# Optimization experiments

Measured on AMD Instinct MI355X. Metric: run time of the kernel, lower is better.

## Reference

```python
import jax, jax.numpy as jnp
import numpy as np

B, C, W, H = 2, 64, 96, 96


def _conv1x1(Wm, b, x):
    # 1x1 conv == per-pixel channel mixing: (O,C) x (B,C,W,H) -> (B,O,W,H)
    return jnp.einsum('oc,bchw->bohw', Wm, x) + b[None, :, None, None]


def setup_inputs() -> dict:
    key = jax.random.key(0)
    ks = jax.random.split(key, 12)
    s = 1.0 / np.sqrt(C)
    inp = {
        'x': jax.random.normal(ks[0], (B, C, W, H), jnp.float32),
        'y': jax.random.normal(ks[1], (B, C, W, H), jnp.float32),
        'Wq': jax.random.normal(ks[2], (C, C), jnp.float32) * s,
        'bq': jax.random.normal(ks[3], (C,), jnp.float32) * 0.01,
        'Wk': jax.random.normal(ks[4], (C, C), jnp.float32) * s,
        'bk': jax.random.normal(ks[5], (C,), jnp.float32) * 0.01,
        'Wvx': jax.random.normal(ks[6], (C, C), jnp.float32) * s,
        'bvx': jax.random.normal(ks[7], (C,), jnp.float32) * 0.01,
        'Wvy': jax.random.normal(ks[8], (C, C), jnp.float32) * s,
        'bvy': jax.random.normal(ks[9], (C,), jnp.float32) * 0.01,
        'gamma': jax.random.normal(ks[10], (1,), jnp.float32) * 0.1,
        'beta': jax.random.normal(ks[11], (1,), jnp.float32) * 0.1,
    }
    return inp


def reference(x, y, Wq, bq, Wk, bk, Wvx, bvx, Wvy, bvy, gamma, beta):
    b, c, w, h = x.shape
    n = w * h
    # Q from y, K from x (cross-query structure of the original module)
    q = _conv1x1(Wq, bq, y).reshape(b, c, n)          # (B,C,N)
    k = _conv1x1(Wk, bk, x).reshape(b, c, n)          # (B,C,N)
    energy = jnp.einsum('bcm,bcn->bmn', q, k)         # (B,N,N), query rows m
    attention = jax.nn.softmax(energy, axis=-1)       # softmax over keys n
    vx = _conv1x1(Wvx, bvx, x).reshape(b, c, n)       # (B,C,N)
    vy = _conv1x1(Wvy, bvy, y).reshape(b, c, n)
    # torch: bmm(value, attention^T) -> out[:, :, m] = sum_n value[:, :, n] * att[m, n]
    out_x = jnp.einsum('bcn,bmn->bcm', vx, attention).reshape(b, c, w, h)
    out_y = jnp.einsum('bcn,bmn->bcm', vy, attention).reshape(b, c, w, h)
    x_att = gamma[0] * out_x
    y_att = beta[0] * out_y
    return (x_att, y_att)
```

## Files before the change

### kernel.cpp

```cpp
#include <hip/hip_runtime.h>
#include <cstdint>
#include <cstddef>

#define BN 2
#define CC 64
#define NN 9216
#define KT 64
#define L2E 1.44269504088896340736f
#define M0L2 63.478581798f
#define PPAD 72

typedef __attribute__((ext_vector_type(8))) _Float16 half8;
typedef __attribute__((ext_vector_type(2))) __fp16 fp16x2;
typedef __attribute__((ext_vector_type(8))) short s16x8;
typedef __attribute__((ext_vector_type(4))) float f32x4;
typedef unsigned short u16;
typedef unsigned int u32;

__device__ __forceinline__ u16 f2h(float f) {
  union { _Float16 h; u16 u; } c; c.h = (_Float16)f; return c.u;
}
__device__ __forceinline__ u32 pack2h(float a, float b) {
  return (u32)f2h(a) | ((u32)f2h(b) << 16);
}
__device__ __forceinline__ u16 f2bf(float f) {
  union { float f; u32 u; } c; c.f = f;
  u32 u = c.u + 0x7FFFu + ((c.u >> 16) & 1u);
  return (u16)(u >> 16);
}
__device__ __forceinline__ half8 cvt8(f32x4 lo, f32x4 hi) {
  union { half8 v; fp16x2 p[4]; } u;
  u.p[0] = __builtin_amdgcn_cvt_pkrtz(lo[0], lo[1]);
  u.p[1] = __builtin_amdgcn_cvt_pkrtz(lo[2], lo[3]);
  u.p[2] = __builtin_amdgcn_cvt_pkrtz(hi[0], hi[1]);
  u.p[3] = __builtin_amdgcn_cvt_pkrtz(hi[2], hi[3]);
  return u.v;
}
__device__ __forceinline__ u32 fbits(float f) {
  union { float f; u32 u; } c; c.f = f; return c.u;
}
__device__ __forceinline__ void cp16(const u16* g, u16* l) {
  __builtin_amdgcn_global_load_lds(
      (const __attribute__((address_space(1))) u32*)g,
      (__attribute__((address_space(3))) u32*)l, 16, 0, 0);
}

__global__ __launch_bounds__(256) void conv_mfma_kernel(
    const float* __restrict__ x, const float* __restrict__ y,
    const float* __restrict__ Wq, const float* __restrict__ bq,
    const float* __restrict__ Wk, const float* __restrict__ bk,
    const float* __restrict__ Wvx, const float* __restrict__ bvx,
    const float* __restrict__ Wvy, const float* __restrict__ bvy,
    u16* __restrict__ qkv) {
  const int cv = blockIdx.y;
  const int b = blockIdx.z;
  const int p0 = blockIdx.x * 128;
  const int tid = threadIdx.x;
  const int lane = tid & 63;
  const int wv = tid >> 6;
  const int l15 = lane & 15;
  const int h = lane >> 4;

  const float* src = (cv == 1 || cv == 2) ? x : y;
  const float* Wm = cv == 0 ? Wq : (cv == 1 ? Wk : (cv == 2 ? Wvx : Wvy));
  const float* bv = cv == 0 ? bq : (cv == 1 ? bk : (cv == 2 ? bvx : bvy));
  u16* dst = qkv + (size_t)cv * ((size_t)BN * NN * CC);

  __shared__ u16 Tr[128 * 72];

  half8 wf[4][2];
#pragma unroll
  for (int ob = 0; ob < 4; ++ob)
#pragma unroll
    for (int kc = 0; kc < 2; ++kc) {
      const float* wr = Wm + (16 * ob + l15) * 64 + 32 * kc + 8 * h;
      wf[ob][kc] = cvt8(*(const f32x4*)wr, *(const f32x4*)(wr + 4));
    }

  f32x4 acc[2][4];
#pragma unroll
  for (int ob = 0; ob < 4; ++ob) {
    f32x4 bias = *(const f32x4*)(bv + 16 * ob + 4 * h);
#pragma unroll
    for (int pt = 0; pt < 2; ++pt) acc[pt][ob] = bias;
  }

  const float* xbase = src + (size_t)b * CC * NN;
#pragma unroll
  for (int pt = 0; pt < 2; ++pt) {
    const int px = p0 + 32 * wv + 16 * pt + l15;
    half8 xf[2];
#pragma unroll
    for (int kc = 0; kc < 2; ++kc) {
      const float* xp = xbase + (size_t)(32 * kc + 8 * h) * NN + px;
      float s[8];
#pragma unroll
      for (int j = 0; j < 8; ++j) s[j] = xp[(size_t)j * NN];
      xf[kc] = cvt8((f32x4){s[0], s[1], s[2], s[3]},
                    (f32x4){s[4], s[5], s[6], s[7]});
    }
#pragma unroll
    for (int ob = 0; ob < 4; ++ob) {
      acc[pt][ob] = __builtin_amdgcn_mfma_f32_16x16x32_f16(wf[ob][0], xf[0], acc[pt][ob], 0, 0, 0);
      acc[pt][ob] = __builtin_amdgcn_mfma_f32_16x16x32_f16(wf[ob][1], xf[1], acc[pt][ob], 0, 0, 0);
    }
  }

  if (cv >= 2) {
#pragma unroll
    for (int pt = 0; pt < 2; ++pt)
#pragma unroll
      for (int ob = 0; ob < 4; ++ob)
#pragma unroll
        for (int r = 0; r < 4; ++r)
          dst[((size_t)b * CC + 16 * ob + 4 * h + r) * NN +
              p0 + 32 * wv + 16 * pt + l15] = f2bf(acc[pt][ob][r]);
  } else {
#pragma unroll
    for (int pt = 0; pt < 2; ++pt) {
      const int pxl = 32 * wv + 16 * pt + l15;
#pragma unroll
      for (int ob = 0; ob < 4; ++ob) {
        uint2 v;
        v.x = pack2h(acc[pt][ob][0], acc[pt][ob][1]);
        v.y = pack2h(acc[pt][ob][2], acc[pt][ob][3]);
        *(uint2*)(Tr + pxl * 72 + 16 * ob + 4 * h) = v;
      }
    }
    __syncthreads();
    const int row = tid >> 1;
    const int hf = tid & 1;
    const uint4* s4 = (const uint4*)(Tr + row * 72) + hf * 4;
    uint4* d4 = (uint4*)(dst + ((size_t)b * NN + p0 + row) * CC) + hf * 4;
#pragma unroll
    for (int i = 0; i < 4; ++i) d4[i] = s4[i];
  }
}

#define TILE_OFF(R, c0) ((((R) * 8) + ((c0) ^ ((R) & 7))) * 8)

template <int SP>
__global__ __launch_bounds__(256, 3) void flash_kernel(
    const u16* __restrict__ qkv, float* __restrict__ accX,
    float* __restrict__ accY, float* __restrict__ ml) {
  constexpr int KPS = NN / SP;
  constexpr int STEPS = KPS / KT;
  const int tid = threadIdx.x;
  const int lane = tid & 63;
  const int wv = tid >> 6;
  const int l15 = lane & 15;
  const int h = lane >> 4;
  const int s = blockIdx.y;
  const int b = blockIdx.z;
  const int m0w = blockIdx.x * 128 + wv * 32;

  const u16* Qt = qkv;
  const u16* Kt = qkv + (size_t)1 * BN * NN * CC;
  const u16* Vx = qkv + (size_t)2 * BN * NN * CC;
  const u16* Vy = qkv + (size_t)3 * BN * NN * CC;

  __shared__ u16 Klds[2][64 * 64];
  __shared__ u16 Vxlds[64 * 64];
  __shared__ u16 Vylds[64 * 64];
  __shared__ u16 Plds[4][32 * PPAD];

  {
    const int n0 = s * KPS;
#pragma unroll
    for (int it = 0; it < 2; ++it) {
      int i = tid + it * 256;
      int r = i >> 3, cc = i & 7;
      int sc = (cc ^ (r & 7)) * 8;
      cp16(Kt + ((size_t)b * NN + n0 + r) * CC + sc, (u16*)Klds[0] + (size_t)i * 8);
    }
  }

  half8 qf[2][2];
#pragma unroll
  for (int mb = 0; mb < 2; ++mb)
#pragma unroll
    for (int ch = 0; ch < 2; ++ch)
      qf[mb][ch] = *(const half8*)(Qt + ((size_t)b * NN + m0w + 16 * mb + l15) * CC +
                                   32 * ch + 8 * h);

  const s16x8 ones = {0x3F80, 0x3F80, 0x3F80, 0x3F80,
                      0x3F80, 0x3F80, 0x3F80, 0x3F80};

  f32x4 oX[4][2], oY[4][2], lacc[2];
#pragma unroll
  for (int cb = 0; cb < 4; ++cb)
#pragma unroll
    for (int mb = 0; mb < 2; ++mb) {
      oX[cb][mb] = (f32x4){0.f, 0.f, 0.f, 0.f};
      oY[cb][mb] = (f32x4){0.f, 0.f, 0.f, 0.f};
    }
#pragma unroll
  for (int mb = 0; mb < 2; ++mb) lacc[mb] = (f32x4){0.f, 0.f, 0.f, 0.f};

  __syncthreads();

  int kb = 0;
#pragma unroll 1
  for (int step = 0; step < STEPS; ++step) {
    const int n0 = s * KPS + step * KT;

#pragma unroll
    for (int it = 0; it < 2; ++it) {
      int i = tid + it * 256;
      int r = i >> 3, cc = i & 7;
      int sc = (cc ^ (r & 7)) * 8;
      cp16(Vx + ((size_t)b * CC + r) * NN + n0 + sc, (u16*)Vxlds + (size_t)i * 8);
      cp16(Vy + ((size_t)b * CC + r) * NN + n0 + sc, (u16*)Vylds + (size_t)i * 8);
    }
    if (step + 1 < STEPS) {
      const int n1 = n0 + KT;
#pragma unroll
      for (int it = 0; it < 2; ++it) {
        int i = tid + it * 256;
        int r = i >> 3, cc = i & 7;
        int sc = (cc ^ (r & 7)) * 8;
        cp16(Kt + ((size_t)b * NN + n1 + r) * CC + sc,
             (u16*)Klds[kb ^ 1] + (size_t)i * 8);
      }
      asm volatile("s_waitcnt vmcnt(6)" ::: "memory");
    } else {
      asm volatile("s_waitcnt vmcnt(4)" ::: "memory");
    }
    __builtin_amdgcn_s_barrier();
    asm volatile("" ::: "memory");

    half8 kf[4][2];
#pragma unroll
    for (int nb = 0; nb < 4; ++nb) {
      int R = 16 * nb + l15;
#pragma unroll
      for (int ch = 0; ch < 2; ++ch)
        kf[nb][ch] = *(const half8*)((const u16*)Klds[kb] + TILE_OFF(R, 4 * ch + h));
    }
    f32x4 st[2][4];
    __builtin_amdgcn_s_setprio(1);
#pragma unroll
    for (int mb = 0; mb < 2; ++mb)
#pragma unroll
      for (int nb = 0; nb < 4; ++nb) {
        f32x4 a = (f32x4){0.f, 0.f, 0.f, 0.f};
        a = __builtin_amdgcn_mfma_f32_16x16x32_f16(kf[nb][0], qf[mb][0], a, 0, 0, 0);
        a = __builtin_amdgcn_mfma_f32_16x16x32_f16(kf[nb][1], qf[mb][1], a, 0, 0, 0);
        st[mb][nb] = a;
      }
    __builtin_amdgcn_s_setprio(0);

#pragma unroll
    for (int mb = 0; mb < 2; ++mb) {
      u32* prow = (u32*)(&Plds[wv][(16 * mb + l15) * PPAD]);
#pragma unroll
      for (int nb = 0; nb < 4; ++nb) {
        u32 u0 = fbits(exp2f(fmaf(st[mb][nb][0], L2E, -M0L2)));
        u32 u1 = fbits(exp2f(fmaf(st[mb][nb][1], L2E, -M0L2)));
        u32 u2 = fbits(exp2f(fmaf(st[mb][nb][2], L2E, -M0L2)));
        u32 u3 = fbits(exp2f(fmaf(st[mb][nb][3], L2E, -M0L2)));
        uint2 v;
        v.x = (u0 >> 16) | (u1 & 0xffff0000u);
        v.y = (u2 >> 16) | (u3 & 0xffff0000u);
        *(uint2*)(prow + 8 * nb + 2 * h) = v;
      }
    }

    asm volatile("s_waitcnt lgkmcnt(0)" ::: "memory");

    s16x8 pf[2][2];
#pragma unroll
    for (int mb = 0; mb < 2; ++mb) {
      int R = 16 * mb + l15;
#pragma unroll
      for (int kc = 0; kc < 2; ++kc)
        pf[mb][kc] = *(const s16x8*)(&Plds[wv][0] + R * PPAD + (4 * kc + h) * 8);
    }

    if (step + 1 < STEPS) {
      asm volatile("s_waitcnt vmcnt(2)" ::: "memory");
    } else {
      asm volatile("s_waitcnt vmcnt(0)" ::: "memory");
    }
    __builtin_amdgcn_s_barrier();
    asm volatile("" ::: "memory");

    __builtin_amdgcn_s_setprio(1);
#pragma unroll
    for (int cb = 0; cb < 4; ++cb) {
      int R = 16 * cb + l15;
#pragma unroll
      for (int kc = 0; kc < 2; ++kc) {
        s16x8 bx = *(const s16x8*)(Vxlds + TILE_OFF(R, 4 * kc + h));
        s16x8 by = *(const s16x8*)(Vylds + TILE_OFF(R, 4 * kc + h));
#pragma unroll
        for (int mb = 0; mb < 2; ++mb) {
          oX[cb][mb] = __builtin_amdgcn_mfma_f32_16x16x32_bf16(pf[mb][kc], bx, oX[cb][mb], 0, 0, 0);
          oY[cb][mb] = __builtin_amdgcn_mfma_f32_16x16x32_bf16(pf[mb][kc], by, oY[cb][mb], 0, 0, 0);
        }
      }
    }
#pragma unroll
    for (int mb = 0; mb < 2; ++mb)
#pragma unroll
      for (int kc = 0; kc < 2; ++kc)
        lacc[mb] = __builtin_amdgcn_mfma_f32_16x16x32_bf16(pf[mb][kc], ones, lacc[mb], 0, 0, 0);
    __builtin_amdgcn_s_setprio(0);

    __builtin_amdgcn_s_barrier();
    asm volatile("" ::: "memory");
    kb ^= 1;
  }

  const size_t bs = (size_t)b * SP + s;
#pragma unroll
  for (int mb = 0; mb < 2; ++mb) {
#pragma unroll
    for (int r = 0; r < 4; ++r) {
      const int m = m0w + 16 * mb + 4 * h + r;
      if (l15 == 0) ml[bs * NN + m] = lacc[mb][r];
#pragma unroll
      for (int cb = 0; cb < 4; ++cb) {
        accX[(bs * NN + m) * CC + 16 * cb + l15] = oX[cb][mb][r];
        accY[(bs * NN + m) * CC + 16 * cb + l15] = oY[cb][mb][r];
      }
    }
  }
}

template <int SP>
__global__ __launch_bounds__(256) void combine_kernel(
    const float* __restrict__ accX, const float* __restrict__ accY,
    const float* __restrict__ ml, const float* __restrict__ gbuf,
    const float* __restrict__ bbuf, float* __restrict__ out) {
  const int tid = threadIdx.x;
  const int b = blockIdx.x / 288;
  const int m0 = (blockIdx.x % 288) * 32;
  __shared__ float lX[64][33];
  __shared__ float lY[64][33];
  {
    const int mi = tid >> 3;
    const int c0 = (tid & 7) * 8;
    const int m = m0 + mi;
    float L = 0.f;
#pragma unroll
    for (int sp = 0; sp < SP; ++sp)
      L += ml[((size_t)b * SP + sp) * NN + m];
    const float invL = 1.0f / L;
    const float ga = gbuf[0] * invL;
    const float be = bbuf[0] * invL;
    f32x4 xv0 = (f32x4){0.f, 0.f, 0.f, 0.f}, xv1 = xv0, yv0 = xv0, yv1 = xv0;
#pragma unroll
    for (int sp = 0; sp < SP; ++sp) {
      size_t off = (((size_t)b * SP + sp) * NN + m) * CC + c0;
      xv0 += *(const f32x4*)(accX + off);
      xv1 += *(const f32x4*)(accX + off + 4);
      yv0 += *(const f32x4*)(accY + off);
      yv1 += *(const f32x4*)(accY + off + 4);
    }
#pragma unroll
    for (int r = 0; r < 4; ++r) {
      lX[c0 + r][mi] = xv0[r] * ga;
      lX[c0 + 4 + r][mi] = xv1[r] * ga;
      lY[c0 + r][mi] = yv0[r] * be;
      lY[c0 + 4 + r][mi] = yv1[r] * be;
    }
  }
  __syncthreads();
  {
    const int c = tid >> 2;
    const int mq = (tid & 3) * 8;
    float* ox = out + ((size_t)b * CC + c) * NN + m0 + mq;
    float* oy = ox + (size_t)BN * CC * NN;
    f32x4 vx0, vx1, vy0, vy1;
#pragma unroll
    for (int r = 0; r < 4; ++r) {
      vx0[r] = lX[c][mq + r];
      vx1[r] = lX[c][mq + 4 + r];
      vy0[r] = lY[c][mq + r];
      vy1[r] = lY[c][mq + 4 + r];
    }
    *(f32x4*)ox = vx0;
    *(f32x4*)(ox + 4) = vx1;
    *(f32x4*)oy = vy0;
    *(f32x4*)(oy + 4) = vy1;
  }
}

extern "C" void kernel_launch(void* const* d_in, const int* in_sizes, int n_in,
                              void* d_out, int out_size, void* d_ws, size_t ws_size,
                              hipStream_t stream) {
  const float* x   = (const float*)d_in[0];
  const float* y   = (const float*)d_in[1];
  const float* Wq  = (const float*)d_in[2];
  const float* bq  = (const float*)d_in[3];
  const float* Wk  = (const float*)d_in[4];
  const float* bk  = (const float*)d_in[5];
  const float* Wvx = (const float*)d_in[6];
  const float* bvx = (const float*)d_in[7];
  const float* Wvy = (const float*)d_in[8];
  const float* bvy = (const float*)d_in[9];
  const float* ga  = (const float*)d_in[10];
  const float* be  = (const float*)d_in[11];

  const size_t qkv_bytes = (size_t)4 * BN * NN * CC * 2;

  conv_mfma_kernel<<<dim3(72, 4, 2), 256, 0, stream>>>(x, y, Wq, bq, Wk, bk,
                                                       Wvx, bvx, Wvy, bvy,
                                                       (u16*)d_ws);

  const size_t acc8 = (size_t)BN * 8 * NN * CC * 4;
  const size_t need8 = qkv_bytes + 2 * acc8 + (size_t)BN * 8 * NN * 4;

  u16* qkv = (u16*)d_ws;
  if (ws_size >= need8) {
    float* accX = (float*)((char*)d_ws + qkv_bytes);
    float* accY = accX + (size_t)BN * 8 * NN * CC;
    float* mlb  = accY + (size_t)BN * 8 * NN * CC;
    flash_kernel<8><<<dim3(72, 8, BN), 256, 0, stream>>>(qkv, accX, accY, mlb);
    combine_kernel<8><<<dim3(576), 256, 0, stream>>>(accX, accY, mlb, ga, be,
                                                     (float*)d_out);
  } else {
    float* accX = (float*)((char*)d_ws + qkv_bytes);
    float* accY = accX + (size_t)BN * 4 * NN * CC;
    float* mlb  = accY + (size_t)BN * 4 * NN * CC;
    flash_kernel<4><<<dim3(72, 4, BN), 256, 0, stream>>>(qkv, accX, accY, mlb);
    combine_kernel<4><<<dim3(576), 256, 0, stream>>>(accX, accY, mlb, ga, be,
                                                     (float*)d_out);
  }
}
```

Baseline: 207.7 us.

## Permute K rows so QK^T MFMA output feeds PV operand directly from registers

Loads K tiles into LDS with a permuted row order, so the score accumulator layout from the QK^T MFMA already matches the A-operand layout the PV MFMA expects. This removes the per-wave P staging buffer in LDS, along with its writes, the lgkmcnt wait and the reads back. The freed LDS and registers allow the occupancy hint to rise from 3 to 5 blocks per CU. Correctness depends on the permutation matching both MFMA layouts exactly, and the higher occupancy target may cause register spills.

```diff
diff --git a/kernel.cpp b/kernel.cpp
--- a/kernel.cpp
+++ b/kernel.cpp
@@ -8,7 +8,6 @@
 #define KT 64
 #define L2E 1.44269504088896340736f
 #define M0L2 63.478581798f
-#define PPAD 72
 
 typedef __attribute__((ext_vector_type(8))) _Float16 half8;
 typedef __attribute__((ext_vector_type(2))) __fp16 fp16x2;
@@ -43,6 +42,9 @@
   __builtin_amdgcn_global_load_lds(
       (const __attribute__((address_space(1))) u32*)g,
       (__attribute__((address_space(3))) u32*)l, 16, 0, 0);
+}
+__device__ __forceinline__ int permk(int r) {
+  return (r & 0x23) | ((r & 0x0C) << 1) | ((r & 0x10) >> 2);
 }
 
 __global__ __launch_bounds__(256) void conv_mfma_kernel(
@@ -140,7 +142,7 @@
 #define TILE_OFF(R, c0) ((((R) * 8) + ((c0) ^ ((R) & 7))) * 8)
 
 template <int SP>
-__global__ __launch_bounds__(256, 3) void flash_kernel(
+__global__ __launch_bounds__(256, 5) void flash_kernel(
     const u16* __restrict__ qkv, float* __restrict__ accX,
     float* __restrict__ accY, float* __restrict__ ml) {
   constexpr int KPS = NN / SP;
@@ -162,7 +164,6 @@
   __shared__ u16 Klds[2][64 * 64];
   __shared__ u16 Vxlds[64 * 64];
   __shared__ u16 Vylds[64 * 64];
-  __shared__ u16 Plds[4][32 * PPAD];
 
   {
     const int n0 = s * KPS;
@@ -171,7 +172,8 @@
       int i = tid + it * 256;
       int r = i >> 3, cc = i & 7;
       int sc = (cc ^ (r & 7)) * 8;
-      cp16(Kt + ((size_t)b * NN + n0 + r) * CC + sc, (u16*)Klds[0] + (size_t)i * 8);
+      cp16(Kt + ((size_t)b * NN + n0 + permk(r)) * CC + sc,
+           (u16*)Klds[0] + (size_t)i * 8);
     }
   }
 
@@ -219,7 +221,7 @@
         int i = tid + it * 256;
         int r = i >> 3, cc = i & 7;
         int sc = (cc ^ (r & 7)) * 8;
-        cp16(Kt + ((size_t)b * NN + n1 + r) * CC + sc,
+        cp16(Kt + ((size_t)b * NN + n1 + permk(r)) * CC + sc,
              (u16*)Klds[kb ^ 1] + (size_t)i * 8);
       }
       asm volatile("s_waitcnt vmcnt(6)" ::: "memory");
@@ -250,31 +252,28 @@
       }
     __builtin_amdgcn_s_setprio(0);
 
+    s16x8 pf[2][2];
 #pragma unroll
     for (int mb = 0; mb < 2; ++mb) {
-      u32* prow = (u32*)(&Plds[wv][(16 * mb + l15) * PPAD]);
+      uint2 pw[4];
 #pragma unroll
       for (int nb = 0; nb < 4; ++nb) {
         u32 u0 = fbits(exp2f(fmaf(st[mb][nb][0], L2E, -M0L2)));
         u32 u1 = fbits(exp2f(fmaf(st[mb][nb][1], L2E, -M0L2)));
         u32 u2 = fbits(exp2f(fmaf(st[mb][nb][2], L2E, -M0L2)));
         u32 u3 = fbits(exp2f(fmaf(st[mb][nb][3], L2E, -M0L2)));
-        uint2 v;
-        v.x = (u0 >> 16) | (u1 & 0xffff0000u);
-        v.y = (u2 >> 16) | (u3 & 0xffff0000u);
-        *(uint2*)(prow + 8 * nb + 2 * h) = v;
-      }
-    }
-
-    asm volatile("s_waitcnt lgkmcnt(0)" ::: "memory");
-
-    s16x8 pf[2][2];
-#pragma unroll
-    for (int mb = 0; mb < 2; ++mb) {
-      int R = 16 * mb + l15;
-#pragma unroll
-      for (int kc = 0; kc < 2; ++kc)
-        pf[mb][kc] = *(const s16x8*)(&Plds[wv][0] + R * PPAD + (4 * kc + h) * 8);
+        pw[nb].x = (u0 >> 16) | (u1 & 0xffff0000u);
+        pw[nb].y = (u2 >> 16) | (u3 & 0xffff0000u);
+      }
+#pragma unroll
+      for (int kc = 0; kc < 2; ++kc) {
+        union { s16x8 v; u32 w[4]; } pu;
+        pu.w[0] = pw[2 * kc].x;
+        pu.w[1] = pw[2 * kc].y;
+        pu.w[2] = pw[2 * kc + 1].x;
+        pu.w[3] = pw[2 * kc + 1].y;
+        pf[mb][kc] = pu.v;
+      }
     }
 
     if (step + 1 < STEPS) {
```

New measurement: 596.6 us. +187.2%, slower.
